# Performance work log

Measured on AMD Instinct MI355X. Metric: run time of the kernel, lower is better.

The kernel has to match this reference:

```python
import jax, jax.numpy as jnp
import numpy as np

NEG_SLOPE = 0.2
EPS = 1e-16


def gat_conv(x, src, dst, W, a_src, a_dst, bias, heads, out_dim):
    """PyG-style GATConv (add_self_loops already applied via src/dst).
    x: [N, F_in]; src/dst: [E] int; W: [F_in, heads*out_dim];
    a_src/a_dst: [heads, out_dim]; bias: [heads*out_dim] or [out_dim].
    Returns [N, heads*out_dim] (concat) or [N, out_dim] when heads==1.
    """
    N = x.shape[0]
    h = (x @ W).reshape(N, heads, out_dim)                     # [N, H, D]
    alpha_src = jnp.einsum('nhd,hd->nh', h, a_src)             # [N, H]
    alpha_dst = jnp.einsum('nhd,hd->nh', h, a_dst)             # [N, H]
    e = jax.nn.leaky_relu(alpha_src[src] + alpha_dst[dst], NEG_SLOPE)  # [E, H]
    # segment softmax over edges grouped by destination node
    m = jax.ops.segment_max(e, dst, num_segments=N)            # [N, H]
    ex = jnp.exp(e - m[dst])                                   # [E, H]
    s = jax.ops.segment_sum(ex, dst, num_segments=N)           # [N, H]
    alpha = ex / (s[dst] + EPS)                                # [E, H]
    msg = h[src] * alpha[:, :, None]                           # [E, H, D]
    out = jax.ops.segment_sum(msg, dst, num_segments=N)        # [N, H, D]
    return out.reshape(N, heads * out_dim) + bias


def setup_inputs() -> dict:
    key = jax.random.key(0)
    ks = jax.random.split(key, 12)
    N, E = 50000, 1600000
    F_in, H, D, C = 128, 8, 8, 40
    x = jax.random.normal(ks[0], (N, F_in), dtype=jnp.float32)
    edge_index = jax.random.randint(ks[1], (2, E), 0, N, dtype=jnp.int32)
    edge_attr = jax.random.normal(ks[2], (E, 1), dtype=jnp.float32)
    # Glorot-ish init for weights, zeros for bias (PyG defaults)
    W1 = jax.random.normal(ks[3], (F_in, H * D), dtype=jnp.float32) * (1.0 / np.sqrt(F_in))
    att_src1 = jax.random.normal(ks[4], (H, D), dtype=jnp.float32) * (1.0 / np.sqrt(D))
    att_dst1 = jax.random.normal(ks[5], (H, D), dtype=jnp.float32) * (1.0 / np.sqrt(D))
    bias1 = jnp.zeros((H * D,), dtype=jnp.float32)
    W2 = jax.random.normal(ks[6], (H * D, C), dtype=jnp.float32) * (1.0 / np.sqrt(H * D))
    att_src2 = jax.random.normal(ks[7], (1, C), dtype=jnp.float32) * (1.0 / np.sqrt(C))
    att_dst2 = jax.random.normal(ks[8], (1, C), dtype=jnp.float32) * (1.0 / np.sqrt(C))
    bias2 = jnp.zeros((C,), dtype=jnp.float32)
    return {"x": x, "edge_index": edge_index, "edge_attr": edge_attr,
            "W1": W1, "att_src1": att_src1, "att_dst1": att_dst1, "bias1": bias1,
            "W2": W2, "att_src2": att_src2, "att_dst2": att_dst2, "bias2": bias2}


def reference(x, edge_index, edge_attr, W1, att_src1, att_dst1, bias1,
              W2, att_src2, att_dst2, bias2):
    N = x.shape[0]
    x = x.astype(jnp.float32)
    edge_attr = edge_attr.astype(jnp.float32)  # cast as original; unused downstream
    # add self-loops (PyG GATConv default add_self_loops=True)
    loop = jnp.arange(N, dtype=edge_index.dtype)
    src = jnp.concatenate([edge_index[0], loop])
    dst = jnp.concatenate([edge_index[1], loop])
    h = gat_conv(x, src, dst, W1, att_src1, att_dst1, bias1, heads=8, out_dim=8)
    h = jax.nn.elu(h)
    out = gat_conv(h, src, dst, W2, att_src2, att_dst2, bias2, heads=1, out_dim=W2.shape[1])
    return out
```

## Files before the change

### kernel.cpp

```cpp
#include <hip/hip_runtime.h>
#include <hip/hip_fp16.h>
#include <cstdint>

#define NEG_SLOPE 0.2f
#define EPSV 1e-16f

#define BIN_SHIFT 7
#define NODES_PER_BIN 128
#define MAXBINS 512
#define CHUNK 2048

typedef _Float16 half8v __attribute__((ext_vector_type(8)));
typedef float float4v __attribute__((ext_vector_type(4)));
typedef int v4i __attribute__((ext_vector_type(4)));
typedef int v2i __attribute__((ext_vector_type(2)));

__device__ float buf_load_f32(v4i rsrc, int voffset, int soffset, int aux) __asm("llvm.amdgcn.raw.buffer.load.f32");
__device__ int   buf_load_i32(v4i rsrc, int voffset, int soffset, int aux) __asm("llvm.amdgcn.raw.buffer.load.i32");
__device__ v2i   buf_load_2xi32(v4i rsrc, int voffset, int soffset, int aux) __asm("llvm.amdgcn.raw.buffer.load.v2i32");

__device__ inline v4i make_rsrc(const void* p, unsigned bytes) {
    union { v4i v; struct { const void* p; unsigned range; unsigned cfg; } s; } u;
    u.s.p = p; u.s.range = bytes; u.s.cfg = 0x00020000u;
    return u.v;
}

__global__ __launch_bounds__(256) void gemm1_alpha(
    const float* __restrict__ x, const float* __restrict__ W1,
    const float* __restrict__ aS, const float* __restrict__ aD,
    __half* __restrict__ h1h, float* __restrict__ as1, float* __restrict__ ad1, int N)
{
    __shared__ _Float16 xh[64 * 128];
    __shared__ _Float16 wt[64 * 128];
    int t = threadIdx.x;
    int n0 = blockIdx.x * 64;

    const float2* x2 = (const float2*)x;
#pragma unroll
    for (int i = 0; i < 16; ++i) {
        int p = t + i * 256;
        int n = p >> 6, kp = p & 63;
        int gn = n0 + n;
        float2 v = (gn < N) ? x2[(size_t)gn * 64 + kp] : make_float2(0.f, 0.f);
        union { _Float16 h[2]; uint32_t u; } cv;
        cv.h[0] = (_Float16)v.x; cv.h[1] = (_Float16)v.y;
        *(uint32_t*)&xh[n * 128 + ((kp * 2) ^ ((n & 7) << 3))] = cv.u;
    }
#pragma unroll
    for (int i = 0; i < 32; ++i) {
        int p = t + i * 256;
        int k = p >> 6, c = p & 63;
        wt[c * 128 + (k ^ ((c & 7) << 3))] = (_Float16)W1[p];
    }
    __syncthreads();

    int wv = t >> 6, l = t & 63;
    int m0 = wv * 16;
    int lr = l & 15;
    int lg = l >> 4;
    float4v acc[4];
#pragma unroll
    for (int ct = 0; ct < 4; ++ct) acc[ct] = (float4v)(0.f);
#pragma unroll
    for (int kt = 0; kt < 4; ++kt) {
        int kh0 = kt * 32 + lg * 8;
        int an = m0 + lr;
        half8v aF = *(half8v*)&xh[an * 128 + (kh0 ^ ((an & 7) << 3))];
#pragma unroll
        for (int ct = 0; ct < 4; ++ct) {
            int c = ct * 16 + lr;
            half8v bF = *(half8v*)&wt[c * 128 + (kh0 ^ ((c & 7) << 3))];
            acc[ct] = __builtin_amdgcn_mfma_f32_16x16x32_f16(aF, bF, acc[ct], 0, 0, 0);
        }
    }
#pragma unroll
    for (int ct = 0; ct < 4; ++ct) {
        int c = ct * 16 + lr;
        float asc = aS[c], adc = aD[c];
#pragma unroll
        for (int i = 0; i < 4; ++i) {
            int n = n0 + m0 + lg * 4 + i;
            float v = acc[ct][i];
            float s = v * asc, d = v * adc;
            s += __shfl_xor(s, 1, 64); s += __shfl_xor(s, 2, 64); s += __shfl_xor(s, 4, 64);
            d += __shfl_xor(d, 1, 64); d += __shfl_xor(d, 2, 64); d += __shfl_xor(d, 4, 64);
            if (n < N) {
                h1h[(size_t)n * 64 + c] = __float2half(v);
                if ((l & 7) == 0) {
                    int hd = 2 * ct + ((l >> 3) & 1);
                    as1[n * 8 + hd] = s;
                    ad1[n * 8 + hd] = d;
                }
            }
        }
    }
}

__global__ __launch_bounds__(256) void binhist(
    const int* __restrict__ dsts, int* __restrict__ offmat, int E, int Et, int nbins, int nb)
{
    __shared__ int lh[MAXBINS];
    int t = threadIdx.x;
    for (int i = t; i < nbins; i += 256) lh[i] = 0;
    __syncthreads();
    int base = blockIdx.x * CHUNK;
#pragma unroll
    for (int r = 0; r < CHUNK / 256; ++r) {
        int i = base + r * 256 + t;
        if (i < Et) {
            int dn = (i < E) ? dsts[i] : (i - E);
            atomicAdd(&lh[dn >> BIN_SHIFT], 1);
        }
    }
    __syncthreads();
    for (int i = t; i < nbins; i += 256)
        offmat[(size_t)i * nb + blockIdx.x] = lh[i];
}

__global__ __launch_bounds__(256) void binscan2(
    int* __restrict__ offmat, int* __restrict__ bincnt, int nb)
{
    __shared__ int tsum[256];
    __shared__ int carry;
    int b = blockIdx.x, t = threadIdx.x;
    int* row = offmat + (size_t)b * nb;
    if (t == 0) carry = 0;
    __syncthreads();
    for (int base = 0; base < nb; base += 1024) {
        int i0 = base + t * 4;
        int v0 = (i0 + 0 < nb) ? row[i0 + 0] : 0;
        int v1 = (i0 + 1 < nb) ? row[i0 + 1] : 0;
        int v2 = (i0 + 2 < nb) ? row[i0 + 2] : 0;
        int v3 = (i0 + 3 < nb) ? row[i0 + 3] : 0;
        int s = v0 + v1 + v2 + v3;
        tsum[t] = s;
        __syncthreads();
        for (int off = 1; off < 256; off <<= 1) {
            int y = (t >= off) ? tsum[t - off] : 0;
            __syncthreads();
            tsum[t] += y;
            __syncthreads();
        }
        int e = tsum[t] - s + carry;
        if (i0 + 0 < nb) row[i0 + 0] = e;        e += v0;
        if (i0 + 1 < nb) row[i0 + 1] = e;        e += v1;
        if (i0 + 2 < nb) row[i0 + 2] = e;        e += v2;
        if (i0 + 3 < nb) row[i0 + 3] = e;
        __syncthreads();
        if (t == 255) carry += tsum[255];
        __syncthreads();
    }
    if (t == 0) bincnt[b] = carry;
}

__global__ __launch_bounds__(256) void binscan(
    const int* __restrict__ bincnt, int* __restrict__ binoff,
    int* __restrict__ row_ptr, int nbins, int N, int Et)
{
    __shared__ int tsum[256];
    int t = threadIdx.x;
    int i0 = t * 2;
    int v0 = (i0 + 0 < nbins) ? bincnt[i0 + 0] : 0;
    int v1 = (i0 + 1 < nbins) ? bincnt[i0 + 1] : 0;
    int s = v0 + v1;
    tsum[t] = s;
    __syncthreads();
    for (int off = 1; off < 256; off <<= 1) {
        int y = (t >= off) ? tsum[t - off] : 0;
        __syncthreads();
        tsum[t] += y;
        __syncthreads();
    }
    int e = tsum[t] - s;
    if (i0 + 0 < nbins) binoff[i0 + 0] = e;  e += v0;
    if (i0 + 1 < nbins) binoff[i0 + 1] = e;
    if (t == 255) binoff[nbins] = tsum[255];
    if (t == 0) row_ptr[N] = Et;
}

__global__ __launch_bounds__(256) void binscatter(
    const int* __restrict__ srcs, const int* __restrict__ dsts,
    const int* __restrict__ binoff, const int* __restrict__ offmat,
    unsigned int* __restrict__ binned, int E, int Et, int nbins, int nb)
{
    __shared__ int gbase[MAXBINS];
    __shared__ int lcur[MAXBINS];
    int t = threadIdx.x, blk = blockIdx.x;
    for (int i = t; i < nbins; i += 256) {
        gbase[i] = binoff[i] + offmat[(size_t)i * nb + blk];
        lcur[i] = 0;
    }
    __syncthreads();
    int base = blk * CHUNK;
#pragma unroll
    for (int r = 0; r < CHUNK / 256; ++r) {
        int i = base + r * 256 + t;
        if (i < Et) {
            int s, dn;
            if (i < E) { s = srcs[i]; dn = dsts[i]; }
            else       { s = i - E;   dn = s; }
            int b = dn >> BIN_SHIFT;
            int li = atomicAdd(&lcur[b], 1);
            binned[gbase[b] + li] = ((unsigned)(dn & (NODES_PER_BIN - 1)) << 24) | (unsigned)s;
        }
    }
}

__global__ __launch_bounds__(256) void binsort(
    const unsigned int* __restrict__ binned, const int* __restrict__ binoff,
    int* __restrict__ row_ptr, int* __restrict__ colx, int N, int nbins)
{
    __shared__ int lh[NODES_PER_BIN];
    __shared__ int lcur[NODES_PER_BIN];
    int b = blockIdx.x, t = threadIdx.x;
    int beg = binoff[b], end = binoff[b + 1];
    if (t < NODES_PER_BIN) lh[t] = 0;
    __syncthreads();
    for (int j = beg + t; j < end; j += 256)
        atomicAdd(&lh[binned[j] >> 24], 1);
    __syncthreads();
    int own = (t < NODES_PER_BIN) ? lh[t] : 0;
    for (int off = 1; off < NODES_PER_BIN; off <<= 1) {
        int y = (t >= off && t < NODES_PER_BIN) ? lh[t - off] : 0;
        __syncthreads();
        if (t < NODES_PER_BIN) lh[t] += y;
        __syncthreads();
    }
    if (t < NODES_PER_BIN) {
        int excl = lh[t] - own;
        int gnode = (b << BIN_SHIFT) + t;
        if (gnode < N) row_ptr[gnode] = beg + excl;
        lcur[t] = excl;
    }
    __syncthreads();
    for (int j = beg + t; j < end; j += 256) {
        unsigned p = binned[j];
        int pos = atomicAdd(&lcur[p >> 24], 1);
        colx[beg + pos] = (int)(p & 0xFFFFFF);
    }
}

__global__ __launch_bounds__(256) void gather1(
    const int* __restrict__ row_ptr, const int* __restrict__ colx,
    const float* __restrict__ as1, const float* __restrict__ ad1,
    const __half* __restrict__ h1h, const float* __restrict__ bias1,
    float* __restrict__ helu, int N)
{
    int wave = (blockIdx.x * 256 + threadIdx.x) >> 6;
    if (wave >= N) return;
    int lane = threadIdx.x & 63;
    int q = lane >> 4;
    int sl = lane & 15;
    int hh = sl >> 1;
    int sl8 = sl << 3;
    v4i rsH = make_rsrc(h1h, (unsigned)N * 128u);
    v4i rsA = make_rsrc(as1, (unsigned)N * 32u);
    int n = wave;
    float adn = ad1[n * 8 + hh];
    int beg = row_ptr[n], end = row_ptr[n + 1];
    float ax = 0.f, ay = 0.f, az = 0.f, aw = 0.f, ws = 0.f;
    int albase = lane >> 3;
    int alhead = (lane & 7) << 2;

    for (int cb = beg; cb < end; cb += 64) {
        int cnt = min(64, end - cb);
        int sv = (cb + lane < end) ? colx[cb + lane] : 0;
        int groups = (cnt + 7) >> 3;
        for (int g = 0; g < groups; ++g) {
            int gk = g << 3;
            int sg = __shfl(sv, gk + albase, 64);
            float aV = buf_load_f32(rsA, (sg << 5) + alhead, 0, 0);
#pragma unroll
            for (int hs = 0; hs < 2; ++hs) {
                int e = (hs << 2) + q;
                int k = gk + e;
                int s = __shfl(sv, k, 64);
                float a = __shfl(aV, (e << 3) + hh, 64);
                v2i hv = buf_load_2xi32(rsH, (s << 7) + sl8, 0, 0);
                float ee = a + adn; ee = fmaxf(ee, NEG_SLOPE * ee);
                float w = (k < cnt) ? __expf(ee) : 0.f;
                union { int i; __half2 h; } u0, u1; u0.i = hv[0]; u1.i = hv[1];
                float2 f0 = __half22float2(u0.h);
                float2 f1 = __half22float2(u1.h);
                ax = fmaf(w, f0.x, ax); ay = fmaf(w, f0.y, ay);
                az = fmaf(w, f1.x, az); aw = fmaf(w, f1.y, aw);
                ws += w;
            }
        }
    }
    ax += __shfl_xor(ax, 16, 64); ax += __shfl_xor(ax, 32, 64);
    ay += __shfl_xor(ay, 16, 64); ay += __shfl_xor(ay, 32, 64);
    az += __shfl_xor(az, 16, 64); az += __shfl_xor(az, 32, 64);
    aw += __shfl_xor(aw, 16, 64); aw += __shfl_xor(aw, 32, 64);
    ws += __shfl_xor(ws, 16, 64); ws += __shfl_xor(ws, 32, 64);
    if (lane < 16) {
        float4 b = ((const float4*)bias1)[sl];
        float inv = 1.f / (ws + EPSV);
        float v0 = ax * inv + b.x;
        float v1 = ay * inv + b.y;
        float v2 = az * inv + b.z;
        float v3 = aw * inv + b.w;
        v0 = (v0 > 0.f) ? v0 : (__expf(v0) - 1.f);
        v1 = (v1 > 0.f) ? v1 : (__expf(v1) - 1.f);
        v2 = (v2 > 0.f) ? v2 : (__expf(v2) - 1.f);
        v3 = (v3 > 0.f) ? v3 : (__expf(v3) - 1.f);
        *(float4*)&helu[(size_t)n * 64 + (sl << 2)] = make_float4(v0, v1, v2, v3);
    }
}

__global__ __launch_bounds__(256) void gemm2_alpha(
    const float* __restrict__ helu, const float* __restrict__ W2,
    const float* __restrict__ aS, const float* __restrict__ aD,
    __half* __restrict__ h2h, float* __restrict__ as2, float* __restrict__ ad2, int N)
{
    __shared__ _Float16 xh[64 * 64];
    __shared__ _Float16 wt[48 * 64];
    int t = threadIdx.x;
    int n0 = blockIdx.x * 64;

    for (int i = t; i < (48 * 64) / 2; i += 256) ((uint32_t*)wt)[i] = 0;
    __syncthreads();

    const float2* h2p = (const float2*)helu;
#pragma unroll
    for (int i = 0; i < 8; ++i) {
        int p = t + i * 256;
        int n = p >> 5, kp = p & 31;
        int gn = n0 + n;
        float2 v = (gn < N) ? h2p[(size_t)gn * 32 + kp] : make_float2(0.f, 0.f);
        union { _Float16 h[2]; uint32_t u; } cv;
        cv.h[0] = (_Float16)v.x; cv.h[1] = (_Float16)v.y;
        *(uint32_t*)&xh[n * 64 + ((kp * 2) ^ ((n & 7) << 3))] = cv.u;
    }
#pragma unroll
    for (int i = 0; i < 10; ++i) {
        int p = t + i * 256;
        if (p < 64 * 40) {
            int k = p / 40, c = p - k * 40;
            wt[c * 64 + (k ^ ((c & 7) << 3))] = (_Float16)W2[p];
        }
    }
    __syncthreads();

    int wv = t >> 6, l = t & 63;
    int m0 = wv * 16;
    int lr = l & 15;
    int lg = l >> 4;
    float4v acc[3];
#pragma unroll
    for (int ct = 0; ct < 3; ++ct) acc[ct] = (float4v)(0.f);
#pragma unroll
    for (int kt = 0; kt < 2; ++kt) {
        int kh0 = kt * 32 + lg * 8;
        int an = m0 + lr;
        half8v aF = *(half8v*)&xh[an * 64 + (kh0 ^ ((an & 7) << 3))];
#pragma unroll
        for (int ct = 0; ct < 3; ++ct) {
            int c = ct * 16 + lr;
            half8v bF = *(half8v*)&wt[c * 64 + (kh0 ^ ((c & 7) << 3))];
            acc[ct] = __builtin_amdgcn_mfma_f32_16x16x32_f16(aF, bF, acc[ct], 0, 0, 0);
        }
    }
    float sv[4] = {0.f, 0.f, 0.f, 0.f};
    float dv[4] = {0.f, 0.f, 0.f, 0.f};
#pragma unroll
    for (int ct = 0; ct < 3; ++ct) {
        int c = ct * 16 + lr;
        bool av = (c < 40);
        float asc = av ? aS[c] : 0.f;
        float adc = av ? aD[c] : 0.f;
#pragma unroll
        for (int i = 0; i < 4; ++i) {
            int n = n0 + m0 + lg * 4 + i;
            float v = acc[ct][i];
            sv[i] = fmaf(v, asc, sv[i]);
            dv[i] = fmaf(v, adc, dv[i]);
            if (av && n < N) h2h[(size_t)n * 64 + c] = __float2half(v);
        }
    }
#pragma unroll
    for (int i = 0; i < 4; ++i) {
        float s = sv[i], d = dv[i];
        s += __shfl_xor(s, 1, 64); s += __shfl_xor(s, 2, 64);
        s += __shfl_xor(s, 4, 64); s += __shfl_xor(s, 8, 64);
        d += __shfl_xor(d, 1, 64); d += __shfl_xor(d, 2, 64);
        d += __shfl_xor(d, 4, 64); d += __shfl_xor(d, 8, 64);
        int n = n0 + m0 + lg * 4 + i;
        if (lr == 0 && n < N) { as2[n] = s; ad2[n] = d; }
    }
}

__global__ __launch_bounds__(256) void gather2(
    const int* __restrict__ row_ptr, const int* __restrict__ colx,
    const float* __restrict__ as2, const float* __restrict__ ad2,
    const __half* __restrict__ h2h, const float* __restrict__ bias2,
    float* __restrict__ out, int N)
{
    int wave = (blockIdx.x * 256 + threadIdx.x) >> 6;
    if (wave >= N) return;
    int lane = threadIdx.x & 63;
    int q = lane >> 4;
    int sl = lane & 15;
    int sl8 = sl << 3;
    v4i rsH = make_rsrc(h2h, (unsigned)N * 128u);
    v4i rsA = make_rsrc(as2, (unsigned)N * 4u);
    int n = wave;
    float adn = ad2[n];
    int beg = row_ptr[n], end = row_ptr[n + 1];
    float ax = 0.f, ay = 0.f, az = 0.f, aw = 0.f, ws = 0.f;

#define G2_BODY(ii) { \
    int k = ((ii) << 2) + q; \
    int s = __shfl(sv, k, 64); \
    float a = __shfl(aV, k, 64); \
    v2i hv = buf_load_2xi32(rsH, (s << 7) + sl8, 0, 0); \
    float ee = a + adn; ee = fmaxf(ee, NEG_SLOPE * ee); \
    float w = (k < cnt) ? __expf(ee) : 0.f; \
    union { int i; __half2 h; } u0, u1; u0.i = hv[0]; u1.i = hv[1]; \
    float2 f0 = __half22float2(u0.h); \
    float2 f1 = __half22float2(u1.h); \
    ax = fmaf(w, f0.x, ax); ay = fmaf(w, f0.y, ay); \
    az = fmaf(w, f1.x, az); aw = fmaf(w, f1.y, aw); \
    ws += w; }

    for (int cb = beg; cb < end; cb += 64) {
        int cnt = min(64, end - cb);
        int sv = (cb + lane < end) ? colx[cb + lane] : 0;
        float aV = buf_load_f32(rsA, sv << 2, 0, 0);
        int iters = (cnt + 3) >> 2;
        int i = 0;
        for (; i + 2 <= iters; i += 2) { G2_BODY(i) G2_BODY(i + 1) }
        for (; i < iters; ++i) { G2_BODY(i) }
    }
#undef G2_BODY

    ax += __shfl_xor(ax, 16, 64); ax += __shfl_xor(ax, 32, 64);
    ay += __shfl_xor(ay, 16, 64); ay += __shfl_xor(ay, 32, 64);
    az += __shfl_xor(az, 16, 64); az += __shfl_xor(az, 32, 64);
    aw += __shfl_xor(aw, 16, 64); aw += __shfl_xor(aw, 32, 64);
    ws += __shfl_xor(ws, 16, 64); ws += __shfl_xor(ws, 32, 64);
    if (lane < 10) {
        float4 b = *(const float4*)&bias2[sl << 2];
        float inv = 1.f / (ws + EPSV);
        *(float4*)&out[(size_t)n * 40 + (sl << 2)] =
            make_float4(ax * inv + b.x, ay * inv + b.y, az * inv + b.z, aw * inv + b.w);
    }
}

extern "C" void kernel_launch(void* const* d_in, const int* in_sizes, int n_in,
                              void* d_out, int out_size, void* d_ws, size_t ws_size,
                              hipStream_t stream)
{
    const float* x   = (const float*)d_in[0];
    const int*   ei  = (const int*)d_in[1];
    const float* W1  = (const float*)d_in[3];
    const float* aS1 = (const float*)d_in[4];
    const float* aD1 = (const float*)d_in[5];
    const float* b1  = (const float*)d_in[6];
    const float* W2  = (const float*)d_in[7];
    const float* aS2 = (const float*)d_in[8];
    const float* aD2 = (const float*)d_in[9];
    const float* b2  = (const float*)d_in[10];

    int N  = in_sizes[0] / 128;
    int E  = in_sizes[1] / 2;
    int Et = E + N;
    int nbins = (N + NODES_PER_BIN - 1) >> BIN_SHIFT;
    int nb = (Et + CHUNK - 1) / CHUNK;

    float* fws   = (float*)d_ws;
    float* as1   = fws;
    float* ad1   = as1  + (size_t)N * 8;
    float* helu  = ad1  + (size_t)N * 8;
    float* as2   = helu + (size_t)N * 64;
    float* ad2   = as2  + (size_t)N;
    __half* h1h  = (__half*)(ad2 + (size_t)N);
    __half* h2h  = h1h + (size_t)N * 64;
    int*   iws     = (int*)(h2h + (size_t)N * 64);
    int*   row_ptr = iws;
    int*   bincnt  = row_ptr + N + 1;
    int*   binoff  = bincnt + MAXBINS + 1;
    int*   offmat  = binoff + MAXBINS + 1;
    unsigned int* binned = (unsigned int*)(offmat + (size_t)MAXBINS * nb);
    int*   colx    = (int*)(binned + Et);
    float* out     = (float*)d_out;

    const int* srcs = ei;
    const int* dsts = ei + E;

    binhist<<<nb, 256, 0, stream>>>(dsts, offmat, E, Et, nbins, nb);
    binscan2<<<nbins, 256, 0, stream>>>(offmat, bincnt, nb);
    binscan<<<1, 256, 0, stream>>>(bincnt, binoff, row_ptr, nbins, N, Et);
    binscatter<<<nb, 256, 0, stream>>>(srcs, dsts, binoff, offmat, binned, E, Et, nbins, nb);
    binsort<<<nbins, 256, 0, stream>>>(binned, binoff, row_ptr, colx, N, nbins);

    gemm1_alpha<<<(N + 63) / 64, 256, 0, stream>>>(x, W1, aS1, aD1, h1h, as1, ad1, N);
    gather1<<<(N * 64 + 255) / 256, 256, 0, stream>>>(row_ptr, colx, as1, ad1,
        h1h, b1, helu, N);

    gemm2_alpha<<<(N + 63) / 64, 256, 0, stream>>>(helu, W2, aS2, aD2, h2h, as2, ad2, N);
    gather2<<<(N * 64 + 255) / 256, 256, 0, stream>>>(row_ptr, colx, as2, ad2,
        h2h, b2, out, N);
}
```

Before: 143.8 us.

## Fuse CSR build into cooperative kernel and merge histogram into GEMM1 launch

The histogram pass now runs as extra blocks of the GEMM1 launch, and the scan, bin-offset, scatter and bin-sort stages are merged into one cooperative kernel that uses grid-wide syncs. CHUNK doubles, so fewer histogram/scatter blocks are needed. The goal is to cut kernel launch overhead and serialization among the small CSR-build kernels and to overlap the histogram with the GEMM. The cooperative launch requires every block to be resident at once, the GEMM kernel's larger shared memory footprint now also applies to the histogram blocks, and the grid syncs carry their own cost.

```diff
diff --git a/kernel.cpp b/kernel.cpp
--- a/kernel.cpp
+++ b/kernel.cpp
@@ -1,6 +1,9 @@
 #include <hip/hip_runtime.h>
 #include <hip/hip_fp16.h>
+#include <hip/hip_cooperative_groups.h>
 #include <cstdint>
+
+namespace cg = cooperative_groups;
 
 #define NEG_SLOPE 0.2f
 #define EPSV 1e-16f
@@ -8,7 +11,7 @@
 #define BIN_SHIFT 7
 #define NODES_PER_BIN 128
 #define MAXBINS 512
-#define CHUNK 2048
+#define CHUNK 4096
 
 typedef _Float16 half8v __attribute__((ext_vector_type(8)));
 typedef float float4v __attribute__((ext_vector_type(4)));
@@ -25,16 +28,38 @@
     return u.v;
 }
 
-__global__ __launch_bounds__(256) void gemm1_alpha(
+__global__ __launch_bounds__(256) void gemm1_hist(
     const float* __restrict__ x, const float* __restrict__ W1,
     const float* __restrict__ aS, const float* __restrict__ aD,
-    __half* __restrict__ h1h, float* __restrict__ as1, float* __restrict__ ad1, int N)
+    __half* __restrict__ h1h, float* __restrict__ as1, float* __restrict__ ad1, int N,
+    const int* __restrict__ dsts, int* __restrict__ offmat,
+    int E, int Et, int nbins, int nb, int gemmBlocks)
 {
     __shared__ _Float16 xh[64 * 128];
     __shared__ _Float16 wt[64 * 128];
+    __shared__ int lhist[MAXBINS];
     int t = threadIdx.x;
+
+    if ((int)blockIdx.x >= gemmBlocks) {
+        int blk = blockIdx.x - gemmBlocks;
+        for (int i = t; i < nbins; i += 256) lhist[i] = 0;
+        __syncthreads();
+        int base = blk * CHUNK;
+#pragma unroll
+        for (int r = 0; r < CHUNK / 256; ++r) {
+            int i = base + r * 256 + t;
+            if (i < Et) {
+                int dn = (i < E) ? dsts[i] : (i - E);
+                atomicAdd(&lhist[dn >> BIN_SHIFT], 1);
+            }
+        }
+        __syncthreads();
+        for (int i = t; i < nbins; i += 256)
+            offmat[(size_t)i * nb + blk] = lhist[i];
+        return;
+    }
+
     int n0 = blockIdx.x * 64;
-
     const float2* x2 = (const float2*)x;
 #pragma unroll
     for (int i = 0; i < 16; ++i) {
@@ -96,43 +121,58 @@
     }
 }
 
-__global__ __launch_bounds__(256) void binhist(
-    const int* __restrict__ dsts, int* __restrict__ offmat, int E, int Et, int nbins, int nb)
+__global__ __launch_bounds__(256) void csr_coop(
+    const int* __restrict__ srcs, const int* __restrict__ dsts,
+    int* __restrict__ offmat, int* __restrict__ bincnt,
+    unsigned int* __restrict__ binned, int* __restrict__ row_ptr, int* __restrict__ colx,
+    int E, int Et, int nbins, int nb, int N)
 {
-    __shared__ int lh[MAXBINS];
-    int t = threadIdx.x;
-    for (int i = t; i < nbins; i += 256) lh[i] = 0;
-    __syncthreads();
-    int base = blockIdx.x * CHUNK;
-#pragma unroll
-    for (int r = 0; r < CHUNK / 256; ++r) {
-        int i = base + r * 256 + t;
-        if (i < Et) {
-            int dn = (i < E) ? dsts[i] : (i - E);
-            atomicAdd(&lh[dn >> BIN_SHIFT], 1);
-        }
-    }
-    __syncthreads();
-    for (int i = t; i < nbins; i += 256)
-        offmat[(size_t)i * nb + blockIdx.x] = lh[i];
-}
-
-__global__ __launch_bounds__(256) void binscan2(
-    int* __restrict__ offmat, int* __restrict__ bincnt, int nb)
-{
+    cg::grid_group grid = cg::this_grid();
     __shared__ int tsum[256];
     __shared__ int carry;
-    int b = blockIdx.x, t = threadIdx.x;
-    int* row = offmat + (size_t)b * nb;
-    if (t == 0) carry = 0;
-    __syncthreads();
-    for (int base = 0; base < nb; base += 1024) {
-        int i0 = base + t * 4;
-        int v0 = (i0 + 0 < nb) ? row[i0 + 0] : 0;
-        int v1 = (i0 + 1 < nb) ? row[i0 + 1] : 0;
-        int v2 = (i0 + 2 < nb) ? row[i0 + 2] : 0;
-        int v3 = (i0 + 3 < nb) ? row[i0 + 3] : 0;
-        int s = v0 + v1 + v2 + v3;
+    __shared__ int boff_s[MAXBINS + 1];
+    __shared__ int gbase[MAXBINS];
+    __shared__ int lcur[MAXBINS];
+    __shared__ int lh[NODES_PER_BIN];
+    int t = threadIdx.x, b = blockIdx.x;
+
+    if (b < nbins) {
+        int* row = offmat + (size_t)b * nb;
+        if (t == 0) carry = 0;
+        __syncthreads();
+        for (int base = 0; base < nb; base += 1024) {
+            int i0 = base + t * 4;
+            int v0 = (i0 + 0 < nb) ? row[i0 + 0] : 0;
+            int v1 = (i0 + 1 < nb) ? row[i0 + 1] : 0;
+            int v2 = (i0 + 2 < nb) ? row[i0 + 2] : 0;
+            int v3 = (i0 + 3 < nb) ? row[i0 + 3] : 0;
+            int s = v0 + v1 + v2 + v3;
+            tsum[t] = s;
+            __syncthreads();
+            for (int off = 1; off < 256; off <<= 1) {
+                int y = (t >= off) ? tsum[t - off] : 0;
+                __syncthreads();
+                tsum[t] += y;
+                __syncthreads();
+            }
+            int e = tsum[t] - s + carry;
+            if (i0 + 0 < nb) row[i0 + 0] = e;        e += v0;
+            if (i0 + 1 < nb) row[i0 + 1] = e;        e += v1;
+            if (i0 + 2 < nb) row[i0 + 2] = e;        e += v2;
+            if (i0 + 3 < nb) row[i0 + 3] = e;
+            __syncthreads();
+            if (t == 255) carry += tsum[255];
+            __syncthreads();
+        }
+        if (t == 0) bincnt[b] = carry;
+    }
+    grid.sync();
+
+    {
+        int i0 = t * 2;
+        int v0 = (i0 + 0 < nbins) ? bincnt[i0 + 0] : 0;
+        int v1 = (i0 + 1 < nbins) ? bincnt[i0 + 1] : 0;
+        int s = v0 + v1;
         tsum[t] = s;
         __syncthreads();
         for (int off = 1; off < 256; off <<= 1) {
@@ -141,103 +181,63 @@
             tsum[t] += y;
             __syncthreads();
         }
-        int e = tsum[t] - s + carry;
-        if (i0 + 0 < nb) row[i0 + 0] = e;        e += v0;
-        if (i0 + 1 < nb) row[i0 + 1] = e;        e += v1;
-        if (i0 + 2 < nb) row[i0 + 2] = e;        e += v2;
-        if (i0 + 3 < nb) row[i0 + 3] = e;
-        __syncthreads();
-        if (t == 255) carry += tsum[255];
-        __syncthreads();
-    }
-    if (t == 0) bincnt[b] = carry;
-}
-
-__global__ __launch_bounds__(256) void binscan(
-    const int* __restrict__ bincnt, int* __restrict__ binoff,
-    int* __restrict__ row_ptr, int nbins, int N, int Et)
-{
-    __shared__ int tsum[256];
-    int t = threadIdx.x;
-    int i0 = t * 2;
-    int v0 = (i0 + 0 < nbins) ? bincnt[i0 + 0] : 0;
-    int v1 = (i0 + 1 < nbins) ? bincnt[i0 + 1] : 0;
-    int s = v0 + v1;
-    tsum[t] = s;
-    __syncthreads();
-    for (int off = 1; off < 256; off <<= 1) {
-        int y = (t >= off) ? tsum[t - off] : 0;
-        __syncthreads();
-        tsum[t] += y;
-        __syncthreads();
-    }
-    int e = tsum[t] - s;
-    if (i0 + 0 < nbins) binoff[i0 + 0] = e;  e += v0;
-    if (i0 + 1 < nbins) binoff[i0 + 1] = e;
-    if (t == 255) binoff[nbins] = tsum[255];
-    if (t == 0) row_ptr[N] = Et;
-}
-
-__global__ __launch_bounds__(256) void binscatter(
-    const int* __restrict__ srcs, const int* __restrict__ dsts,
-    const int* __restrict__ binoff, const int* __restrict__ offmat,
-    unsigned int* __restrict__ binned, int E, int Et, int nbins, int nb)
-{
-    __shared__ int gbase[MAXBINS];
-    __shared__ int lcur[MAXBINS];
-    int t = threadIdx.x, blk = blockIdx.x;
-    for (int i = t; i < nbins; i += 256) {
-        gbase[i] = binoff[i] + offmat[(size_t)i * nb + blk];
-        lcur[i] = 0;
-    }
-    __syncthreads();
-    int base = blk * CHUNK;
-#pragma unroll
-    for (int r = 0; r < CHUNK / 256; ++r) {
-        int i = base + r * 256 + t;
-        if (i < Et) {
-            int s, dn;
-            if (i < E) { s = srcs[i]; dn = dsts[i]; }
-            else       { s = i - E;   dn = s; }
-            int b = dn >> BIN_SHIFT;
-            int li = atomicAdd(&lcur[b], 1);
-            binned[gbase[b] + li] = ((unsigned)(dn & (NODES_PER_BIN - 1)) << 24) | (unsigned)s;
-        }
-    }
-}
-
-__global__ __launch_bounds__(256) void binsort(
-    const unsigned int* __restrict__ binned, const int* __restrict__ binoff,
-    int* __restrict__ row_ptr, int* __restrict__ colx, int N, int nbins)
-{
-    __shared__ int lh[NODES_PER_BIN];
-    __shared__ int lcur[NODES_PER_BIN];
-    int b = blockIdx.x, t = threadIdx.x;
-    int beg = binoff[b], end = binoff[b + 1];
-    if (t < NODES_PER_BIN) lh[t] = 0;
-    __syncthreads();
-    for (int j = beg + t; j < end; j += 256)
-        atomicAdd(&lh[binned[j] >> 24], 1);
-    __syncthreads();
-    int own = (t < NODES_PER_BIN) ? lh[t] : 0;
-    for (int off = 1; off < NODES_PER_BIN; off <<= 1) {
-        int y = (t >= off && t < NODES_PER_BIN) ? lh[t - off] : 0;
-        __syncthreads();
-        if (t < NODES_PER_BIN) lh[t] += y;
-        __syncthreads();
-    }
-    if (t < NODES_PER_BIN) {
-        int excl = lh[t] - own;
-        int gnode = (b << BIN_SHIFT) + t;
-        if (gnode < N) row_ptr[gnode] = beg + excl;
-        lcur[t] = excl;
-    }
-    __syncthreads();
-    for (int j = beg + t; j < end; j += 256) {
-        unsigned p = binned[j];
-        int pos = atomicAdd(&lcur[p >> 24], 1);
-        colx[beg + pos] = (int)(p & 0xFFFFFF);
-    }
+        int e = tsum[t] - s;
+        if (i0 + 0 < nbins) boff_s[i0 + 0] = e;
+        if (i0 + 1 < nbins) boff_s[i0 + 1] = e + v0;
+        if (t == 255) boff_s[nbins] = tsum[255];
+        __syncthreads();
+    }
+
+    if (b < nb) {
+        for (int i = t; i < nbins; i += 256) {
+            gbase[i] = boff_s[i] + offmat[(size_t)i * nb + b];
+            lcur[i] = 0;
+        }
+        __syncthreads();
+        int base = b * CHUNK;
+#pragma unroll
+        for (int r = 0; r < CHUNK / 256; ++r) {
+            int i = base + r * 256 + t;
+            if (i < Et) {
+                int s, dn;
+                if (i < E) { s = srcs[i]; dn = dsts[i]; }
+                else       { s = i - E;   dn = s; }
+                int bb = dn >> BIN_SHIFT;
+                int li = atomicAdd(&lcur[bb], 1);
+                binned[gbase[bb] + li] = ((unsigned)(dn & (NODES_PER_BIN - 1)) << 24) | (unsigned)s;
+            }
+        }
+    }
+    grid.sync();
+
+    if (b < nbins) {
+        int beg = boff_s[b], end = boff_s[b + 1];
+        if (t < NODES_PER_BIN) lh[t] = 0;
+        __syncthreads();
+        for (int j = beg + t; j < end; j += 256)
+            atomicAdd(&lh[binned[j] >> 24], 1);
+        __syncthreads();
+        int own = (t < NODES_PER_BIN) ? lh[t] : 0;
+        for (int off = 1; off < NODES_PER_BIN; off <<= 1) {
+            int y = (t >= off && t < NODES_PER_BIN) ? lh[t - off] : 0;
+            __syncthreads();
+            if (t < NODES_PER_BIN) lh[t] += y;
+            __syncthreads();
+        }
+        if (t < NODES_PER_BIN) {
+            int excl = lh[t] - own;
+            int gnode = (b << BIN_SHIFT) + t;
+            if (gnode < N) row_ptr[gnode] = beg + excl;
+            lcur[t] = excl;
+        }
+        __syncthreads();
+        for (int j = beg + t; j < end; j += 256) {
+            unsigned p = binned[j];
+            int pos = atomicAdd(&lcur[p >> 24], 1);
+            colx[beg + pos] = (int)(p & 0xFFFFFF);
+        }
+    }
+    if (b == 0 && t == 0) row_ptr[N] = Et;
 }
 
 __global__ __launch_bounds__(256) void gather1(
@@ -488,13 +488,22 @@
     const int* srcs = ei;
     const int* dsts = ei + E;
 
-    binhist<<<nb, 256, 0, stream>>>(dsts, offmat, E, Et, nbins, nb);
-    binscan2<<<nbins, 256, 0, stream>>>(offmat, bincnt, nb);
-    binscan<<<1, 256, 0, stream>>>(bincnt, binoff, row_ptr, nbins, N, Et);
-    binscatter<<<nb, 256, 0, stream>>>(srcs, dsts, binoff, offmat, binned, E, Et, nbins, nb);
-    binsort<<<nbins, 256, 0, stream>>>(binned, binoff, row_ptr, colx, N, nbins);
-
-    gemm1_alpha<<<(N + 63) / 64, 256, 0, stream>>>(x, W1, aS1, aD1, h1h, as1, ad1, N);
+    int gemmBlocks = (N + 63) / 64;
+
+    gemm1_hist<<<gemmBlocks + nb, 256, 0, stream>>>(
+        x, W1, aS1, aD1, h1h, as1, ad1, N, dsts, offmat, E, Et, nbins, nb, gemmBlocks);
+
+    {
+        int coopBlocks = (nb > nbins) ? nb : nbins;
+        void* args[] = {
+            (void*)&srcs, (void*)&dsts, (void*)&offmat, (void*)&bincnt,
+            (void*)&binned, (void*)&row_ptr, (void*)&colx,
+            (void*)&E, (void*)&Et, (void*)&nbins, (void*)&nb, (void*)&N
+        };
+        hipLaunchCooperativeKernel((const void*)csr_coop, dim3(coopBlocks), dim3(256),
+                                   args, 0, stream);
+    }
+
     gather1<<<(N * 64 + 255) / 256, 256, 0, stream>>>(row_ptr, colx, as1, ad1,
         h1h, b1, helu, N);
 
```

Result: slower. 250.0 us (+73.9%).
